# Kernel optimization log

Hardware: AMD Instinct MI355X
Metric: run time of the kernel (lower is better)

The kernel has to match this reference:

```python
import jax, jax.numpy as jnp
import numpy as np

SIGMA = 0.248
PRNUM = 6
P = 7.5
K = 3.0
ALPHA = 2.5


def _gauss_kernel():
    # 5x5 normalized Gaussian, replicated per channel for depthwise conv [O=3,I=1,5,5]
    x = jnp.arange(-2, 3, dtype=jnp.float32)
    x2, y2 = jnp.meshgrid(x, x, indexing='xy')
    k = jnp.exp(-(x2 ** 2 + y2 ** 2) / (2.0 * SIGMA ** 2))
    k = k / jnp.sum(k)
    return jnp.broadcast_to(k[None, None], (3, 1, 5, 5))


def _dwconv(x, k):
    # x: [3,H,W]; depthwise 5x5 conv, padding=2 (matches F.conv2d(..., padding=2, groups=3))
    return jax.lax.conv_general_dilated(
        x[None], k, window_strides=(1, 1), padding=[(2, 2), (2, 2)],
        feature_group_count=3, dimension_numbers=('NCHW', 'OIHW', 'NCHW'))[0]


def _down2(x):
    # torch bilinear align_corners=False at exact scale 0.5 == 2x2 average pooling
    c, h, w = x.shape
    return x.reshape(c, h // 2, 2, w // 2, 2).mean(axis=(2, 4))


def _up(x, hw):
    # torch bilinear align_corners=False upsample (half-pixel centers) == jax linear resize
    return jax.image.resize(x, (x.shape[0], hw[0], hw[1]), method='linear')


def _foveate(img, fixs):
    C, H, W = img.shape
    k = _gauss_kernel()
    # build Gaussian pyramid
    G = img
    pyr = [G]
    for _ in range(1, PRNUM):
        G = _down2(_dwconv(G, k))
        pyr.append(G)
    # re-expand each level back to full res (interpolate then blur at each step)
    As = [pyr[0]]
    for i in range(1, PRNUM):
        cur = pyr[i]
        for j in range(i):
            hw = (cur.shape[1] * 2, cur.shape[2] * 2) if j < i - 1 else (H, W)
            cur = _dwconv(_up(cur, hw), k)
        As.append(cur)
    As = jnp.stack(As)  # [prNum, 3, H, W]

    # radial eccentricity map (min distance over fixations)
    x = jnp.arange(W, dtype=jnp.float32)
    y = jnp.arange(H, dtype=jnp.float32)
    x2d, y2d = jnp.meshgrid(x, y, indexing='xy')  # each [H, W]
    d = jnp.sqrt((x2d[None] - fixs[:, 0, None, None]) ** 2 +
                 (y2d[None] - fixs[:, 1, None, None]) ** 2) / P
    theta = jnp.min(d, axis=0)
    R = ALPHA / (theta + ALPHA)

    Ts = [jnp.exp(-((2.0 ** (i - 3)) * R / SIGMA) ** 2 * K) for i in range(1, PRNUM)]
    Ts.append(jnp.zeros_like(R))

    om = np.minimum(np.sqrt(np.log(2.0) / K) / (2.0 ** np.arange(-2, 3)) * SIGMA, 1.0)
    omega = np.concatenate([om, [0.0]]).astype(np.float32)  # [prNum]

    layer_ind = jnp.zeros_like(R)
    for i in range(1, PRNUM):
        ind = (R >= omega[i]) & (R <= omega[i - 1])
        layer_ind = jnp.where(ind, jnp.float32(i), layer_ind)

    Bs = [(0.5 - Ts[i]) / (Ts[i - 1] - Ts[i] + 1e-5) for i in range(1, PRNUM)]

    Ms = []
    for i in range(PRNUM):
        base = jnp.ones_like(R) if i == 0 else 1.0 - Bs[i - 1]
        M = jnp.where(layer_ind == i, base, jnp.float32(0.0))
        if i < PRNUM - 1:
            M = jnp.where(layer_ind == i + 1, Bs[i], M)
        Ms.append(M)
    Ms = jnp.stack(Ms)  # [prNum, H, W]

    # blend: sum_p Ms[p] * As[p, c]
    im_fov = jnp.einsum('phw,pchw->chw', Ms, As)
    return im_fov


def setup_inputs() -> dict:
    key = jax.random.key(0)
    k1, k2 = jax.random.split(key)
    img = jax.random.uniform(k1, (3, 2048, 2048), dtype=jnp.float32) * 255.0
    fixs = jax.random.uniform(k2, (4, 2), dtype=jnp.float32) * 2048.0
    return {'img': img, 'fixs': fixs}


def reference(img, fixs):
    return _foveate(img, fixs)
```

## Files before the change

### kernel.cpp

```cpp
#include <hip/hip_runtime.h>
#include <math.h>

#define HW2048 (2048ull*2048ull)
typedef float f4 __attribute__((ext_vector_type(4)));
typedef float f2 __attribute__((ext_vector_type(2)));

struct BP {
  float P[4][3];
  float D2[5];
  float cc[5];
};

__global__ __launch_bounds__(256) void downAll_k(const float* __restrict__ img,
                                                 float* __restrict__ C1,
                                                 float* __restrict__ p2,
                                                 float* __restrict__ p3,
                                                 float* __restrict__ p4,
                                                 float* __restrict__ p5) {
  __shared__ float t2[16][17];
  __shared__ float t3[8][9];
  __shared__ float t4a[4][5];
  int tx = threadIdx.x, ty = threadIdx.y;
  int X = blockIdx.x * 16 + tx;
  int Y = blockIdx.y * 16 + ty;
  int c = blockIdx.z;
  const float* ip = img + (size_t)c * HW2048 + (size_t)(4 * Y) * 2048 + 4 * X;
  f4 r0 = __builtin_nontemporal_load((const f4*)(ip));
  f4 r1 = __builtin_nontemporal_load((const f4*)(ip + 2048));
  f4 r2 = __builtin_nontemporal_load((const f4*)(ip + 4096));
  f4 r3 = __builtin_nontemporal_load((const f4*)(ip + 6144));
  float a00 = 0.25f * (r0.x + r0.y + r1.x + r1.y);
  float a01 = 0.25f * (r0.z + r0.w + r1.z + r1.w);
  float a10 = 0.25f * (r2.x + r2.y + r3.x + r3.y);
  float a11 = 0.25f * (r2.z + r2.w + r3.z + r3.w);
  float* cp = C1 + (size_t)c * 1048576 + (size_t)(2 * Y) * 1024 + 2 * X;
  f2 u; u.x = a00; u.y = a01; *(f2*)cp = u;
  f2 v; v.x = a10; v.y = a11; *(f2*)(cp + 1024) = v;
  float m = 0.25f * (a00 + a01 + a10 + a11);
  p2[((size_t)c * 512 + Y) * 512 + X] = m;
  t2[ty][tx] = m;
  __syncthreads();
  int tid = ty * 16 + tx;
  if (tid < 64) {
    int y = tid >> 3, x = tid & 7;
    float w = 0.25f * (t2[2*y][2*x] + t2[2*y][2*x+1] + t2[2*y+1][2*x] + t2[2*y+1][2*x+1]);
    p3[((size_t)c * 256 + blockIdx.y * 8 + y) * 256 + blockIdx.x * 8 + x] = w;
    t3[y][x] = w;
  }
  __syncthreads();
  if (tid < 16) {
    int y = tid >> 2, x = tid & 3;
    float w = 0.25f * (t3[2*y][2*x] + t3[2*y][2*x+1] + t3[2*y+1][2*x] + t3[2*y+1][2*x+1]);
    p4[((size_t)c * 128 + blockIdx.y * 4 + y) * 128 + blockIdx.x * 4 + x] = w;
    t4a[y][x] = w;
  }
  __syncthreads();
  if (tid < 4) {
    int y = tid >> 1, x = tid & 1;
    float w = 0.25f * (t4a[2*y][2*x] + t4a[2*y][2*x+1] + t4a[2*y+1][2*x] + t4a[2*y+1][2*x+1]);
    p5[((size_t)c * 64 + blockIdx.y * 2 + y) * 64 + blockIdx.x * 2 + x] = w;
  }
}

__device__ __forceinline__ void up_coords(int o, int n, int& i0, int& i1, float& w0) {
  int m = o >> 1;
  if (o & 1) { i0 = m; i1 = min(m + 1, n - 1); w0 = 0.75f; }
  else       { i0 = max(m - 1, 0); i1 = m;     w0 = 0.25f; }
}

__global__ __launch_bounds__(1024) void upchain_k(const float* __restrict__ p3,
                                                  const float* __restrict__ p4,
                                                  const float* __restrict__ p5,
                                                  float* __restrict__ U3,
                                                  float* __restrict__ U4,
                                                  float* __restrict__ U5) {
  __shared__ float a[19][20];
  __shared__ float mid[34][35];
  int z = blockIdx.z, im = z / 3, ch = z - im * 3;
  int X0 = blockIdx.x * 64, Y0 = blockIdx.y * 64;
  int tid = threadIdx.x;
  int bx1 = X0 / 4 - 1, by1 = Y0 / 4 - 1;
  int bx2 = X0 / 2 - 1, by2 = Y0 / 2 - 1;

  if (im == 2) {
    const float* s = p5 + ch * 4096;
    for (int j = tid; j < 18 * 18; j += 1024) {
      int r = j / 18, cc = j % 18;
      int gy = min(max(by1 + r, 0), 127), gx = min(max(bx1 + cc, 0), 127);
      int r0, r1, c0, c1; float wy0, wx0;
      up_coords(gy, 64, r0, r1, wy0);
      up_coords(gx, 64, c0, c1, wx0);
      float wy1 = 1.f - wy0, wx1 = 1.f - wx0;
      a[r][cc] = wy0 * (wx0 * s[r0*64+c0] + wx1 * s[r0*64+c1])
               + wy1 * (wx0 * s[r1*64+c0] + wx1 * s[r1*64+c1]);
    }
    __syncthreads();
    for (int j = tid; j < 34 * 34; j += 1024) {
      int r = j / 34, cc = j % 34;
      int gy = min(max(by2 + r, 0), 255), gx = min(max(bx2 + cc, 0), 255);
      int r0, r1, c0, c1; float wy0, wx0;
      up_coords(gy, 128, r0, r1, wy0);
      up_coords(gx, 128, c0, c1, wx0);
      float wy1 = 1.f - wy0, wx1 = 1.f - wx0;
      int a0 = r0 - by1, a1 = r1 - by1, b0 = c0 - bx1, b1 = c1 - bx1;
      mid[r][cc] = wy0 * (wx0 * a[a0][b0] + wx1 * a[a0][b1])
                 + wy1 * (wx0 * a[a1][b0] + wx1 * a[a1][b1]);
    }
    __syncthreads();
  } else if (im == 1) {
    const float* s = p4 + ch * 16384;
    for (int j = tid; j < 34 * 34; j += 1024) {
      int r = j / 34, cc = j % 34;
      int gy = min(max(by2 + r, 0), 255), gx = min(max(bx2 + cc, 0), 255);
      int r0, r1, c0, c1; float wy0, wx0;
      up_coords(gy, 128, r0, r1, wy0);
      up_coords(gx, 128, c0, c1, wx0);
      float wy1 = 1.f - wy0, wx1 = 1.f - wx0;
      mid[r][cc] = wy0 * (wx0 * s[r0*128+c0] + wx1 * s[r0*128+c1])
                 + wy1 * (wx0 * s[r1*128+c0] + wx1 * s[r1*128+c1]);
    }
    __syncthreads();
  }

  float* dst = (im == 0) ? U3 : (im == 1) ? U4 : U5;
  const float* p3g = p3 + ch * 65536;
  int lx = tid & 63, lyb = tid >> 6;
#pragma unroll
  for (int rr = 0; rr < 4; ++rr) {
    int ly = lyb * 4 + rr;
    int x = X0 + lx, y = Y0 + ly;
    int r0, r1, c0, c1; float wy0, wx0;
    up_coords(y, 256, r0, r1, wy0);
    up_coords(x, 256, c0, c1, wx0);
    float wy1 = 1.f - wy0, wx1 = 1.f - wx0;
    float v;
    if (im == 0) {
      v = wy0 * (wx0 * p3g[r0*256+c0] + wx1 * p3g[r0*256+c1])
        + wy1 * (wx0 * p3g[r1*256+c0] + wx1 * p3g[r1*256+c1]);
    } else {
      int a0 = r0 - by2, a1 = r1 - by2, b0 = c0 - bx2, b1 = c1 - bx2;
      v = wy0 * (wx0 * mid[a0][b0] + wx1 * mid[a0][b1])
        + wy1 * (wx0 * mid[a1][b0] + wx1 * mid[a1][b1]);
    }
    dst[((size_t)ch * 512 + y) * 512 + x] = v;
  }
}

__device__ __forceinline__ void s2c(const float* __restrict__ b, int x0, int y0,
                                    const BP& bp, float o[2][4]) {
  int t = x0 >> 2, ky = y0 >> 2, yph = y0 & 3;
  int c[3], r[3];
#pragma unroll
  for (int j = 0; j < 3; ++j) {
    c[j] = min(max(t - 1 + j, 0), 511);
    r[j] = min(max(ky - 1 + j, 0), 511);
  }
  float v[3][3];
#pragma unroll
  for (int j = 0; j < 3; ++j) {
    const float* row = b + r[j] * 512;
    v[j][0] = row[c[0]]; v[j][1] = row[c[1]]; v[j][2] = row[c[2]];
  }
  const float* wr0 = bp.P[yph];
  const float* wr1 = bp.P[yph + 1];
  float rv0[3], rv1[3];
#pragma unroll
  for (int i = 0; i < 3; ++i) {
    rv0[i] = wr0[0] * v[0][i] + wr0[1] * v[1][i] + wr0[2] * v[2][i];
    rv1[i] = wr1[0] * v[0][i] + wr1[1] * v[1][i] + wr1[2] * v[2][i];
  }
#pragma unroll
  for (int p = 0; p < 4; ++p) {
    o[0][p] = bp.P[p][0] * rv0[0] + bp.P[p][1] * rv0[1] + bp.P[p][2] * rv0[2];
    o[1][p] = bp.P[p][0] * rv1[0] + bp.P[p][1] * rv1[1] + bp.P[p][2] * rv1[2];
  }
}

__device__ __forceinline__ void s1c(const float* __restrict__ b, int x0, int y0,
                                    float o[2][4]) {
  int q0 = x0 >> 1, qy = y0 >> 1;
  int c[4], r[3];
#pragma unroll
  for (int i = 0; i < 4; ++i) c[i] = min(max(q0 - 1 + i, 0), 1023);
#pragma unroll
  for (int j = 0; j < 3; ++j) r[j] = min(max(qy - 1 + j, 0), 1023);
  float v[3][4];
#pragma unroll
  for (int j = 0; j < 3; ++j) {
    const float* row = b + r[j] * 1024;
    v[j][0] = row[c[0]]; v[j][1] = row[c[1]]; v[j][2] = row[c[2]]; v[j][3] = row[c[3]];
  }
  float rv0[4], rv1[4];
#pragma unroll
  for (int i = 0; i < 4; ++i) {
    rv0[i] = 0.25f * v[0][i] + 0.75f * v[1][i];
    rv1[i] = 0.75f * v[1][i] + 0.25f * v[2][i];
  }
  o[0][0] = 0.25f * rv0[0] + 0.75f * rv0[1];
  o[0][1] = 0.75f * rv0[1] + 0.25f * rv0[2];
  o[0][2] = 0.25f * rv0[1] + 0.75f * rv0[2];
  o[0][3] = 0.75f * rv0[2] + 0.25f * rv0[3];
  o[1][0] = 0.25f * rv1[0] + 0.75f * rv1[1];
  o[1][1] = 0.75f * rv1[1] + 0.25f * rv1[2];
  o[1][2] = 0.25f * rv1[1] + 0.75f * rv1[2];
  o[1][3] = 0.75f * rv1[2] + 0.25f * rv1[3];
}

__device__ __forceinline__ void sample_level(int l, int x0, int y0,
    const float* __restrict__ imgc, const float* __restrict__ C1c,
    const float* __restrict__ b2, const float* __restrict__ b3,
    const float* __restrict__ b4, const float* __restrict__ b5,
    const BP& bp, float o[2][4]) {
  if (l == 0) {
    f4 v0 = *(const f4*)(imgc + (size_t)y0 * 2048 + x0);
    f4 v1 = *(const f4*)(imgc + (size_t)(y0 + 1) * 2048 + x0);
    o[0][0] = v0.x; o[0][1] = v0.y; o[0][2] = v0.z; o[0][3] = v0.w;
    o[1][0] = v1.x; o[1][1] = v1.y; o[1][2] = v1.z; o[1][3] = v1.w;
  } else if (l == 1) {
    s1c(C1c, x0, y0, o);
  } else {
    const float* b = (l == 2) ? b2 : (l == 3) ? b3 : (l == 4) ? b4 : b5;
    s2c(b, x0, y0, bp, o);
  }
}

__global__ __launch_bounds__(256) void fblend_k(
    const float* __restrict__ img, const float* __restrict__ C1,
    const float* __restrict__ B2, const float* __restrict__ B3,
    const float* __restrict__ B4, const float* __restrict__ B5,
    const float* __restrict__ fixs, int nf,
    float* __restrict__ out, BP bp) {
  int xs = blockIdx.x * 64 + threadIdx.x;
  int yp = blockIdx.y * 4 + threadIdx.y;
  int x0 = xs * 4, y0 = yp * 2;
  size_t ob0 = (size_t)y0 * 2048 + x0;

  float d2[2][4];
#pragma unroll
  for (int j = 0; j < 2; ++j)
#pragma unroll
    for (int i = 0; i < 4; ++i) d2[j][i] = 3.4e38f;
  for (int f = 0; f < nf; ++f) {
    float dx0 = (float)x0 - fixs[2 * f], dy0 = (float)y0 - fixs[2 * f + 1];
#pragma unroll
    for (int j = 0; j < 2; ++j) {
      float dy = dy0 + (float)j, dy2 = dy * dy;
#pragma unroll
      for (int i = 0; i < 4; ++i) {
        float dx = dx0 + (float)i;
        d2[j][i] = fminf(d2[j][i], dx * dx + dy2);
      }
    }
  }

  float dmn = d2[0][0], dmx = d2[0][0];
#pragma unroll
  for (int j = 0; j < 2; ++j)
#pragma unroll
    for (int i = 0; i < 4; ++i) {
      dmn = fminf(dmn, d2[j][i]);
      dmx = fmaxf(dmx, d2[j][i]);
    }
  int lmax = (dmx >= bp.D2[0]) + (dmx >= bp.D2[1]) + (dmx >= bp.D2[2]) +
             (dmx >= bp.D2[3]) + (dmx >= bp.D2[4]);

  if (lmax == 0) {
#pragma unroll
    for (int ch = 0; ch < 3; ++ch) {
      const float* imgc = img + (size_t)ch * HW2048;
      f4 v0 = *(const f4*)(imgc + ob0);
      f4 v1 = *(const f4*)(imgc + ob0 + 2048);
      __builtin_nontemporal_store(v0, (f4*)(out + (size_t)ch * HW2048 + ob0));
      __builtin_nontemporal_store(v1, (f4*)(out + (size_t)ch * HW2048 + ob0 + 2048));
    }
    return;
  }

  int lmin = (dmn >= bp.D2[0]) + (dmn >= bp.D2[1]) + (dmn >= bp.D2[2]) +
             (dmn >= bp.D2[3]) + (dmn >= bp.D2[4]);
  bool mixed = (lmin != lmax);

  float thr  = (lmax == 1) ? bp.D2[0] : (lmax == 2) ? bp.D2[1] :
               (lmax == 3) ? bp.D2[2] : (lmax == 4) ? bp.D2[3] : bp.D2[4];
  float cm_A = (lmax == 1) ? bp.cc[0] : (lmax == 2) ? bp.cc[1] :
               (lmax == 3) ? bp.cc[2] : (lmax == 4) ? bp.cc[3] : bp.cc[4];
  float cm_B = (lmax <= 2) ? bp.cc[0] : (lmax == 3) ? bp.cc[1] :
               (lmax == 4) ? bp.cc[2] : bp.cc[3];
  bool top5 = (lmax >= 5);

  float Bv[2][4];
  bool  tp[2][4];
#pragma unroll
  for (int j = 0; j < 2; ++j)
#pragma unroll
    for (int i = 0; i < 4; ++i) {
      float dd = d2[j][i];
      bool top = (dd >= thr);
      tp[j][i] = top;
      float d = dd * __frsqrt_rn(dd);
      float R = 18.75f * __frcp_rn(d + 18.75f);
      float R2 = R * R;
      float cm = top ? cm_A : cm_B;
      float tsm = __expf(-cm * R2);
      float t2 = tsm * tsm;
      float tsL = (top && top5) ? 0.f : t2 * t2;
      float B = (0.5f - tsL) * __frcp_rn(tsm - tsL + 1e-5f);
      if (!top && lmax == 1) B = 0.f;
      Bv[j][i] = B;
    }

#pragma unroll
  for (int ch = 0; ch < 3; ++ch) {
    const float* imgc = img + (size_t)ch * HW2048;
    const float* C1c  = C1 + (size_t)ch * 1048576;
    const float* b2   = B2 + (size_t)ch * 262144;
    const float* b3   = B3 + (size_t)ch * 262144;
    const float* b4   = B4 + (size_t)ch * 262144;
    const float* b5   = B5 + (size_t)ch * 262144;

    float sA[2][4];
    float sB[2][4];
    float sC[2][4];
    sample_level(lmax,     x0, y0, imgc, C1c, b2, b3, b4, b5, bp, sA);
    sample_level(lmax - 1, x0, y0, imgc, C1c, b2, b3, b4, b5, bp, sB);
#pragma unroll
    for (int j = 0; j < 2; ++j)
#pragma unroll
      for (int i = 0; i < 4; ++i) sC[j][i] = sB[j][i];
    if (mixed && lmax >= 2)
      sample_level(lmax - 2, x0, y0, imgc, C1c, b2, b3, b4, b5, bp, sC);

    float res[2][4];
#pragma unroll
    for (int j = 0; j < 2; ++j)
#pragma unroll
      for (int i = 0; i < 4; ++i) {
        float B = Bv[j][i];
        bool top = tp[j][i];
        float hi = top ? sA[j][i] : sB[j][i];
        float lo = top ? sB[j][i] : sC[j][i];
        res[j][i] = B * lo + (1.f - B) * hi;
      }

    f4 v0, v1;
    v0.x = res[0][0]; v0.y = res[0][1]; v0.z = res[0][2]; v0.w = res[0][3];
    v1.x = res[1][0]; v1.y = res[1][1]; v1.z = res[1][2]; v1.w = res[1][3];
    __builtin_nontemporal_store(v0, (f4*)(out + (size_t)ch * HW2048 + ob0));
    __builtin_nontemporal_store(v1, (f4*)(out + (size_t)ch * HW2048 + ob0 + 2048));
  }
}

extern "C" void kernel_launch(void* const* d_in, const int* in_sizes, int n_in,
                              void* d_out, int out_size, void* d_ws, size_t ws_size,
                              hipStream_t stream) {
  const float* img  = (const float*)d_in[0];
  const float* fixs = (const float*)d_in[1];
  int nf = in_sizes[1] / 2;
  float* out = (float*)d_out;
  float* ws  = (float*)d_ws;

  BP bp;
  const double sig = 0.248, Kd = 3.0, Pd = 7.5, Ad = 2.5;
  double obv = sqrt(log(2.0) / Kd) * sig;
  for (int j = 0; j < 5; ++j) {
    double om = obv * pow(2.0, 2 - j);
    double Dj = Pd * Ad * (1.0 / om - 1.0);
    bp.D2[j] = (float)(Dj * Dj);
  }
  for (int X = 0; X < 5; ++X)
    bp.cc[X] = (float)(Kd * pow(2.0, 2.0 * (X - 2)) / (sig * sig));
  const float Pt[4][3] = {{0.375f, 0.625f, 0.f},
                          {0.1875f, 0.75f, 0.0625f},
                          {0.0625f, 0.75f, 0.1875f},
                          {0.f, 0.625f, 0.375f}};
  for (int a = 0; a < 4; ++a) for (int t = 0; t < 3; ++t) bp.P[a][t] = Pt[a][t];

  size_t o = 0;
  float* C1 = ws + o; o += 3ull * 1024 * 1024;
  float* p2 = ws + o; o += 3ull * 512 * 512;
  float* p3 = ws + o; o += 3ull * 256 * 256;
  float* p4 = ws + o; o += 3ull * 128 * 128;
  float* p5 = ws + o; o += 3ull * 64 * 64;
  float* U3 = ws + o; o += 3ull * 512 * 512;
  float* U4 = ws + o; o += 3ull * 512 * 512;
  float* U5 = ws + o; o += 3ull * 512 * 512;

  downAll_k <<<dim3(32, 32, 3), dim3(16, 16), 0, stream>>>(img, C1, p2, p3, p4, p5);
  upchain_k <<<dim3(8, 8, 9),   dim3(1024),   0, stream>>>(p3, p4, p5, U3, U4, U5);
  fblend_k  <<<dim3(8, 256),    dim3(64, 4),  0, stream>>>(img, C1, p2, U3, U4, U5,
                                                           fixs, nf, out, bp);
}
```

Baseline: 131.1 us.

## Fuse upsample chain into blend kernel via per-block LDS tiles

Removes the separate upchain kernel and its U3/U4/U5 intermediate buffers. Each blend block now computes the needed 512-res upsampled tiles of levels 3-5 directly into shared memory from p3/p4/p5, and only for the levels its block-wide distance bounds say it needs. A block-level eccentricity bound also lets blocks with a single uniform level skip the per-pixel level test. This saves one launch and global round-trips, at the cost of redundant halo computation, more LDS use per block and extra barriers.

```diff
diff --git a/kernel.cpp b/kernel.cpp
--- a/kernel.cpp
+++ b/kernel.cpp
@@ -10,6 +10,11 @@
   float D2[5];
   float cc[5];
 };
+
+__device__ __forceinline__ int ladder5(float dd, const BP& bp) {
+  return (dd >= bp.D2[0]) + (dd >= bp.D2[1]) + (dd >= bp.D2[2]) +
+         (dd >= bp.D2[3]) + (dd >= bp.D2[4]);
+}
 
 __global__ __launch_bounds__(256) void downAll_k(const float* __restrict__ img,
                                                  float* __restrict__ C1,
@@ -68,84 +73,6 @@
   else       { i0 = max(m - 1, 0); i1 = m;     w0 = 0.25f; }
 }
 
-__global__ __launch_bounds__(1024) void upchain_k(const float* __restrict__ p3,
-                                                  const float* __restrict__ p4,
-                                                  const float* __restrict__ p5,
-                                                  float* __restrict__ U3,
-                                                  float* __restrict__ U4,
-                                                  float* __restrict__ U5) {
-  __shared__ float a[19][20];
-  __shared__ float mid[34][35];
-  int z = blockIdx.z, im = z / 3, ch = z - im * 3;
-  int X0 = blockIdx.x * 64, Y0 = blockIdx.y * 64;
-  int tid = threadIdx.x;
-  int bx1 = X0 / 4 - 1, by1 = Y0 / 4 - 1;
-  int bx2 = X0 / 2 - 1, by2 = Y0 / 2 - 1;
-
-  if (im == 2) {
-    const float* s = p5 + ch * 4096;
-    for (int j = tid; j < 18 * 18; j += 1024) {
-      int r = j / 18, cc = j % 18;
-      int gy = min(max(by1 + r, 0), 127), gx = min(max(bx1 + cc, 0), 127);
-      int r0, r1, c0, c1; float wy0, wx0;
-      up_coords(gy, 64, r0, r1, wy0);
-      up_coords(gx, 64, c0, c1, wx0);
-      float wy1 = 1.f - wy0, wx1 = 1.f - wx0;
-      a[r][cc] = wy0 * (wx0 * s[r0*64+c0] + wx1 * s[r0*64+c1])
-               + wy1 * (wx0 * s[r1*64+c0] + wx1 * s[r1*64+c1]);
-    }
-    __syncthreads();
-    for (int j = tid; j < 34 * 34; j += 1024) {
-      int r = j / 34, cc = j % 34;
-      int gy = min(max(by2 + r, 0), 255), gx = min(max(bx2 + cc, 0), 255);
-      int r0, r1, c0, c1; float wy0, wx0;
-      up_coords(gy, 128, r0, r1, wy0);
-      up_coords(gx, 128, c0, c1, wx0);
-      float wy1 = 1.f - wy0, wx1 = 1.f - wx0;
-      int a0 = r0 - by1, a1 = r1 - by1, b0 = c0 - bx1, b1 = c1 - bx1;
-      mid[r][cc] = wy0 * (wx0 * a[a0][b0] + wx1 * a[a0][b1])
-                 + wy1 * (wx0 * a[a1][b0] + wx1 * a[a1][b1]);
-    }
-    __syncthreads();
-  } else if (im == 1) {
-    const float* s = p4 + ch * 16384;
-    for (int j = tid; j < 34 * 34; j += 1024) {
-      int r = j / 34, cc = j % 34;
-      int gy = min(max(by2 + r, 0), 255), gx = min(max(bx2 + cc, 0), 255);
-      int r0, r1, c0, c1; float wy0, wx0;
-      up_coords(gy, 128, r0, r1, wy0);
-      up_coords(gx, 128, c0, c1, wx0);
-      float wy1 = 1.f - wy0, wx1 = 1.f - wx0;
-      mid[r][cc] = wy0 * (wx0 * s[r0*128+c0] + wx1 * s[r0*128+c1])
-                 + wy1 * (wx0 * s[r1*128+c0] + wx1 * s[r1*128+c1]);
-    }
-    __syncthreads();
-  }
-
-  float* dst = (im == 0) ? U3 : (im == 1) ? U4 : U5;
-  const float* p3g = p3 + ch * 65536;
-  int lx = tid & 63, lyb = tid >> 6;
-#pragma unroll
-  for (int rr = 0; rr < 4; ++rr) {
-    int ly = lyb * 4 + rr;
-    int x = X0 + lx, y = Y0 + ly;
-    int r0, r1, c0, c1; float wy0, wx0;
-    up_coords(y, 256, r0, r1, wy0);
-    up_coords(x, 256, c0, c1, wx0);
-    float wy1 = 1.f - wy0, wx1 = 1.f - wx0;
-    float v;
-    if (im == 0) {
-      v = wy0 * (wx0 * p3g[r0*256+c0] + wx1 * p3g[r0*256+c1])
-        + wy1 * (wx0 * p3g[r1*256+c0] + wx1 * p3g[r1*256+c1]);
-    } else {
-      int a0 = r0 - by2, a1 = r1 - by2, b0 = c0 - bx2, b1 = c1 - bx2;
-      v = wy0 * (wx0 * mid[a0][b0] + wx1 * mid[a0][b1])
-        + wy1 * (wx0 * mid[a1][b0] + wx1 * mid[a1][b1]);
-    }
-    dst[((size_t)ch * 512 + y) * 512 + x] = v;
-  }
-}
-
 __device__ __forceinline__ void s2c(const float* __restrict__ b, int x0, int y0,
                                     const BP& bp, float o[2][4]) {
   int t = x0 >> 2, ky = y0 >> 2, yph = y0 & 3;
@@ -160,6 +87,29 @@
   for (int j = 0; j < 3; ++j) {
     const float* row = b + r[j] * 512;
     v[j][0] = row[c[0]]; v[j][1] = row[c[1]]; v[j][2] = row[c[2]];
+  }
+  const float* wr0 = bp.P[yph];
+  const float* wr1 = bp.P[yph + 1];
+  float rv0[3], rv1[3];
+#pragma unroll
+  for (int i = 0; i < 3; ++i) {
+    rv0[i] = wr0[0] * v[0][i] + wr0[1] * v[1][i] + wr0[2] * v[2][i];
+    rv1[i] = wr1[0] * v[0][i] + wr1[1] * v[1][i] + wr1[2] * v[2][i];
+  }
+#pragma unroll
+  for (int p = 0; p < 4; ++p) {
+    o[0][p] = bp.P[p][0] * rv0[0] + bp.P[p][1] * rv0[1] + bp.P[p][2] * rv0[2];
+    o[1][p] = bp.P[p][0] * rv1[0] + bp.P[p][1] * rv1[1] + bp.P[p][2] * rv1[2];
+  }
+}
+
+__device__ __forceinline__ void s2c_lds(const float (*t)[68], int tx, int kyr, int yph,
+                                        const BP& bp, float o[2][4]) {
+  float v[3][3];
+#pragma unroll
+  for (int j = 0; j < 3; ++j) {
+    const float* row = t[kyr + j];
+    v[j][0] = row[tx]; v[j][1] = row[tx + 1]; v[j][2] = row[tx + 2];
   }
   const float* wr0 = bp.P[yph];
   const float* wr1 = bp.P[yph + 1];
@@ -206,65 +156,58 @@
   o[1][3] = 0.75f * rv1[2] + 0.25f * rv1[3];
 }
 
-__device__ __forceinline__ void sample_level(int l, int x0, int y0,
-    const float* __restrict__ imgc, const float* __restrict__ C1c,
-    const float* __restrict__ b2, const float* __restrict__ b3,
-    const float* __restrict__ b4, const float* __restrict__ b5,
-    const BP& bp, float o[2][4]) {
+__device__ __forceinline__ void sampleL(
+    int l, int ch, int x0, int y0, int tx, int kyr,
+    const float* __restrict__ img, const float* __restrict__ C1,
+    const float* __restrict__ p2,
+    const float (*tU)[3][4][68], const BP& bp, float o[2][4]) {
   if (l == 0) {
+    const float* imgc = img + (size_t)ch * HW2048;
     f4 v0 = *(const f4*)(imgc + (size_t)y0 * 2048 + x0);
     f4 v1 = *(const f4*)(imgc + (size_t)(y0 + 1) * 2048 + x0);
     o[0][0] = v0.x; o[0][1] = v0.y; o[0][2] = v0.z; o[0][3] = v0.w;
     o[1][0] = v1.x; o[1][1] = v1.y; o[1][2] = v1.z; o[1][3] = v1.w;
   } else if (l == 1) {
-    s1c(C1c, x0, y0, o);
+    s1c(C1 + (size_t)ch * 1048576, x0, y0, o);
+  } else if (l == 2) {
+    s2c(p2 + (size_t)ch * 262144, x0, y0, bp, o);
   } else {
-    const float* b = (l == 2) ? b2 : (l == 3) ? b3 : (l == 4) ? b4 : b5;
-    s2c(b, x0, y0, bp, o);
+    s2c_lds(tU[ch][l - 3], tx, kyr, y0 & 3, bp, o);
   }
 }
 
 __global__ __launch_bounds__(256) void fblend_k(
     const float* __restrict__ img, const float* __restrict__ C1,
-    const float* __restrict__ B2, const float* __restrict__ B3,
-    const float* __restrict__ B4, const float* __restrict__ B5,
+    const float* __restrict__ p2, const float* __restrict__ p3,
+    const float* __restrict__ p4, const float* __restrict__ p5,
     const float* __restrict__ fixs, int nf,
     float* __restrict__ out, BP bp) {
-  int xs = blockIdx.x * 64 + threadIdx.x;
-  int yp = blockIdx.y * 4 + threadIdx.y;
+  __shared__ float tU[3][3][4][68];
+  __shared__ float tM[3][2][5][38];
+  __shared__ float tA[3][5][22];
+
+  int tx = threadIdx.x, ty = threadIdx.y;
+  int bx = blockIdx.x, by = blockIdx.y;
+  int xs = bx * 64 + tx;
+  int yp = by * 4 + ty;
   int x0 = xs * 4, y0 = yp * 2;
   size_t ob0 = (size_t)y0 * 2048 + x0;
 
-  float d2[2][4];
-#pragma unroll
-  for (int j = 0; j < 2; ++j)
-#pragma unroll
-    for (int i = 0; i < 4; ++i) d2[j][i] = 3.4e38f;
+  int X0 = bx * 256, Y0 = by * 8;
+  float bDmin = 3.4e38f, bDmax = 3.4e38f;
   for (int f = 0; f < nf; ++f) {
-    float dx0 = (float)x0 - fixs[2 * f], dy0 = (float)y0 - fixs[2 * f + 1];
-#pragma unroll
-    for (int j = 0; j < 2; ++j) {
-      float dy = dy0 + (float)j, dy2 = dy * dy;
-#pragma unroll
-      for (int i = 0; i < 4; ++i) {
-        float dx = dx0 + (float)i;
-        d2[j][i] = fminf(d2[j][i], dx * dx + dy2);
-      }
-    }
-  }
-
-  float dmn = d2[0][0], dmx = d2[0][0];
-#pragma unroll
-  for (int j = 0; j < 2; ++j)
-#pragma unroll
-    for (int i = 0; i < 4; ++i) {
-      dmn = fminf(dmn, d2[j][i]);
-      dmx = fmaxf(dmx, d2[j][i]);
-    }
-  int lmax = (dmx >= bp.D2[0]) + (dmx >= bp.D2[1]) + (dmx >= bp.D2[2]) +
-             (dmx >= bp.D2[3]) + (dmx >= bp.D2[4]);
-
-  if (lmax == 0) {
+    float fx = fixs[2 * f], fy = fixs[2 * f + 1];
+    float dxm = fmaxf(fmaxf((float)X0 - fx, fx - (float)(X0 + 255)), 0.f);
+    float dym = fmaxf(fmaxf((float)Y0 - fy, fy - (float)(Y0 + 7)), 0.f);
+    bDmin = fminf(bDmin, dxm * dxm + dym * dym);
+    float dxM = fmaxf(fx - (float)X0, (float)(X0 + 255) - fx);
+    float dyM = fmaxf(fy - (float)Y0, (float)(Y0 + 7) - fy);
+    bDmax = fminf(bDmax, dxM * dxM + dyM * dyM);
+  }
+  int bLmax = ladder5(bDmax + 2.0f, bp);
+  int bLmin = ladder5(fmaxf(bDmin - 2.0f, 0.f), bp);
+
+  if (bLmax == 0) {
 #pragma unroll
     for (int ch = 0; ch < 3; ++ch) {
       const float* imgc = img + (size_t)ch * HW2048;
@@ -276,9 +219,141 @@
     return;
   }
 
-  int lmin = (dmn >= bp.D2[0]) + (dmn >= bp.D2[1]) + (dmn >= bp.D2[2]) +
-             (dmn >= bp.D2[3]) + (dmn >= bp.D2[4]);
-  bool mixed = (lmin != lmax);
+  int sLo = max(bLmin - 1, 3), sHi = min(bLmax, 5);
+  int g0 = 2 * by - 1, c0 = 64 * bx - 1;
+  if (sLo <= sHi) {
+    int m0 = (g0 >> 1) - 1, n0 = (c0 >> 1) - 1;
+    int q0 = (m0 >> 1) - 1, s0 = (n0 >> 1) - 1;
+    int tid = ty * 64 + tx;
+    bool lv5 = (sHi == 5), lv4 = (sLo <= 4 && sHi >= 4), lv3 = (sLo == 3);
+    if (lv5) {
+      for (int i = tid; i < 300; i += 256) {
+        int ch = i / 100, k = i - ch * 100, r = k / 20, cI = k - r * 20;
+        int gy = min(max(q0 + r, 0), 127), gx = min(max(s0 + cI, 0), 127);
+        int r0, r1, e0, e1; float wy0, wx0;
+        up_coords(gy, 64, r0, r1, wy0);
+        up_coords(gx, 64, e0, e1, wx0);
+        float wy1 = 1.f - wy0, wx1 = 1.f - wx0;
+        const float* s = p5 + ch * 4096;
+        tA[ch][r][cI] = wy0 * (wx0 * s[r0*64+e0] + wx1 * s[r0*64+e1])
+                      + wy1 * (wx0 * s[r1*64+e0] + wx1 * s[r1*64+e1]);
+      }
+    }
+    if (lv4) {
+      for (int i = tid; i < 540; i += 256) {
+        int ch = i / 180, k = i - ch * 180, r = k / 36, cI = k - r * 36;
+        int gy = min(max(m0 + r, 0), 255), gx = min(max(n0 + cI, 0), 255);
+        int r0, r1, e0, e1; float wy0, wx0;
+        up_coords(gy, 128, r0, r1, wy0);
+        up_coords(gx, 128, e0, e1, wx0);
+        float wy1 = 1.f - wy0, wx1 = 1.f - wx0;
+        const float* s = p4 + ch * 16384;
+        tM[ch][0][r][cI] = wy0 * (wx0 * s[r0*128+e0] + wx1 * s[r0*128+e1])
+                         + wy1 * (wx0 * s[r1*128+e0] + wx1 * s[r1*128+e1]);
+      }
+    }
+    if (lv3) {
+      for (int i = tid; i < 792; i += 256) {
+        int ch = i / 264, k = i - ch * 264, r = k / 66, cI = k - r * 66;
+        int gy = min(max(g0 + r, 0), 511), gx = min(max(c0 + cI, 0), 511);
+        int r0, r1, e0, e1; float wy0, wx0;
+        up_coords(gy, 256, r0, r1, wy0);
+        up_coords(gx, 256, e0, e1, wx0);
+        float wy1 = 1.f - wy0, wx1 = 1.f - wx0;
+        const float* s = p3 + ch * 65536;
+        tU[ch][0][r][cI] = wy0 * (wx0 * s[r0*256+e0] + wx1 * s[r0*256+e1])
+                         + wy1 * (wx0 * s[r1*256+e0] + wx1 * s[r1*256+e1]);
+      }
+    }
+    __syncthreads();
+    if (lv5) {
+      for (int i = tid; i < 540; i += 256) {
+        int ch = i / 180, k = i - ch * 180, r = k / 36, cI = k - r * 36;
+        int gy = min(max(m0 + r, 0), 255), gx = min(max(n0 + cI, 0), 255);
+        int r0, r1, e0, e1; float wy0, wx0;
+        up_coords(gy, 128, r0, r1, wy0);
+        up_coords(gx, 128, e0, e1, wx0);
+        float wy1 = 1.f - wy0, wx1 = 1.f - wx0;
+        tM[ch][1][r][cI] = wy0 * (wx0 * tA[ch][r0-q0][e0-s0] + wx1 * tA[ch][r0-q0][e1-s0])
+                         + wy1 * (wx0 * tA[ch][r1-q0][e0-s0] + wx1 * tA[ch][r1-q0][e1-s0]);
+      }
+    }
+    if (lv4) {
+      for (int i = tid; i < 792; i += 256) {
+        int ch = i / 264, k = i - ch * 264, r = k / 66, cI = k - r * 66;
+        int gy = min(max(g0 + r, 0), 511), gx = min(max(c0 + cI, 0), 511);
+        int r0, r1, e0, e1; float wy0, wx0;
+        up_coords(gy, 256, r0, r1, wy0);
+        up_coords(gx, 256, e0, e1, wx0);
+        float wy1 = 1.f - wy0, wx1 = 1.f - wx0;
+        tU[ch][1][r][cI] = wy0 * (wx0 * tM[ch][0][r0-m0][e0-n0] + wx1 * tM[ch][0][r0-m0][e1-n0])
+                         + wy1 * (wx0 * tM[ch][0][r1-m0][e0-n0] + wx1 * tM[ch][0][r1-m0][e1-n0]);
+      }
+    }
+    __syncthreads();
+    if (lv5) {
+      for (int i = tid; i < 792; i += 256) {
+        int ch = i / 264, k = i - ch * 264, r = k / 66, cI = k - r * 66;
+        int gy = min(max(g0 + r, 0), 511), gx = min(max(c0 + cI, 0), 511);
+        int r0, r1, e0, e1; float wy0, wx0;
+        up_coords(gy, 256, r0, r1, wy0);
+        up_coords(gx, 256, e0, e1, wx0);
+        float wy1 = 1.f - wy0, wx1 = 1.f - wx0;
+        tU[ch][2][r][cI] = wy0 * (wx0 * tM[ch][1][r0-m0][e0-n0] + wx1 * tM[ch][1][r0-m0][e1-n0])
+                         + wy1 * (wx0 * tM[ch][1][r1-m0][e0-n0] + wx1 * tM[ch][1][r1-m0][e1-n0]);
+      }
+    }
+    __syncthreads();
+  }
+
+  float d2[2][4];
+#pragma unroll
+  for (int j = 0; j < 2; ++j)
+#pragma unroll
+    for (int i = 0; i < 4; ++i) d2[j][i] = 3.4e38f;
+  for (int f = 0; f < nf; ++f) {
+    float dx0 = (float)x0 - fixs[2 * f], dy0 = (float)y0 - fixs[2 * f + 1];
+#pragma unroll
+    for (int j = 0; j < 2; ++j) {
+      float dy = dy0 + (float)j, dy2 = dy * dy;
+#pragma unroll
+      for (int i = 0; i < 4; ++i) {
+        float dx = dx0 + (float)i;
+        d2[j][i] = fminf(d2[j][i], dx * dx + dy2);
+      }
+    }
+  }
+
+  bool uniformB = (bLmin == bLmax);
+  int lmax;
+  bool mixed;
+  if (uniformB) {
+    lmax = bLmax; mixed = false;
+  } else {
+    float dmn = d2[0][0], dmx = d2[0][0];
+#pragma unroll
+    for (int j = 0; j < 2; ++j)
+#pragma unroll
+      for (int i = 0; i < 4; ++i) {
+        dmn = fminf(dmn, d2[j][i]);
+        dmx = fmaxf(dmx, d2[j][i]);
+      }
+    lmax = ladder5(dmx, bp);
+    int lmin = ladder5(dmn, bp);
+    mixed = (lmin != lmax);
+  }
+
+  if (lmax == 0) {
+#pragma unroll
+    for (int ch = 0; ch < 3; ++ch) {
+      const float* imgc = img + (size_t)ch * HW2048;
+      f4 v0 = *(const f4*)(imgc + ob0);
+      f4 v1 = *(const f4*)(imgc + ob0 + 2048);
+      __builtin_nontemporal_store(v0, (f4*)(out + (size_t)ch * HW2048 + ob0));
+      __builtin_nontemporal_store(v1, (f4*)(out + (size_t)ch * HW2048 + ob0 + 2048));
+    }
+    return;
+  }
 
   float thr  = (lmax == 1) ? bp.D2[0] : (lmax == 2) ? bp.D2[1] :
                (lmax == 3) ? bp.D2[2] : (lmax == 4) ? bp.D2[3] : bp.D2[4];
@@ -295,7 +370,7 @@
 #pragma unroll
     for (int i = 0; i < 4; ++i) {
       float dd = d2[j][i];
-      bool top = (dd >= thr);
+      bool top = uniformB ? true : (dd >= thr);
       tp[j][i] = top;
       float d = dd * __frsqrt_rn(dd);
       float R = 18.75f * __frcp_rn(d + 18.75f);
@@ -309,26 +384,18 @@
       Bv[j][i] = B;
     }
 
+  int kyr = ty >> 1;
 #pragma unroll
   for (int ch = 0; ch < 3; ++ch) {
-    const float* imgc = img + (size_t)ch * HW2048;
-    const float* C1c  = C1 + (size_t)ch * 1048576;
-    const float* b2   = B2 + (size_t)ch * 262144;
-    const float* b3   = B3 + (size_t)ch * 262144;
-    const float* b4   = B4 + (size_t)ch * 262144;
-    const float* b5   = B5 + (size_t)ch * 262144;
-
-    float sA[2][4];
-    float sB[2][4];
-    float sC[2][4];
-    sample_level(lmax,     x0, y0, imgc, C1c, b2, b3, b4, b5, bp, sA);
-    sample_level(lmax - 1, x0, y0, imgc, C1c, b2, b3, b4, b5, bp, sB);
+    float sA[2][4], sB[2][4], sC[2][4];
+    sampleL(lmax,     ch, x0, y0, tx, kyr, img, C1, p2, tU, bp, sA);
+    sampleL(lmax - 1, ch, x0, y0, tx, kyr, img, C1, p2, tU, bp, sB);
 #pragma unroll
     for (int j = 0; j < 2; ++j)
 #pragma unroll
       for (int i = 0; i < 4; ++i) sC[j][i] = sB[j][i];
     if (mixed && lmax >= 2)
-      sample_level(lmax - 2, x0, y0, imgc, C1c, b2, b3, b4, b5, bp, sC);
+      sampleL(lmax - 2, ch, x0, y0, tx, kyr, img, C1, p2, tU, bp, sC);
 
     float res[2][4];
 #pragma unroll
@@ -381,12 +448,8 @@
   float* p3 = ws + o; o += 3ull * 256 * 256;
   float* p4 = ws + o; o += 3ull * 128 * 128;
   float* p5 = ws + o; o += 3ull * 64 * 64;
-  float* U3 = ws + o; o += 3ull * 512 * 512;
-  float* U4 = ws + o; o += 3ull * 512 * 512;
-  float* U5 = ws + o; o += 3ull * 512 * 512;
 
   downAll_k <<<dim3(32, 32, 3), dim3(16, 16), 0, stream>>>(img, C1, p2, p3, p4, p5);
-  upchain_k <<<dim3(8, 8, 9),   dim3(1024),   0, stream>>>(p3, p4, p5, U3, U4, U5);
-  fblend_k  <<<dim3(8, 256),    dim3(64, 4),  0, stream>>>(img, C1, p2, U3, U4, U5,
+  fblend_k  <<<dim3(8, 256),    dim3(64, 4),  0, stream>>>(img, C1, p2, p3, p4, p5,
                                                            fixs, nf, out, bp);
 }
```

After: 132.5 us. No clear change (+1.1%).
